# Performance work log

Measured on AMD Instinct MI355X. Metric: run time of the kernel, lower is better.

The kernel has to match this reference:

```python
import jax, jax.numpy as jnp
import numpy as np

E = 1024
H = 16
D = E // H  # projection_dim = 64


def setup_inputs() -> dict:
    key = jax.random.key(0)
    ks = jax.random.split(key, 9)
    s = 1.0 / np.sqrt(E)
    return {
        "inputs": jax.random.normal(ks[0], (2, 2048, E), dtype=jnp.float32),
        "Wq": jax.random.uniform(ks[1], (E, E), jnp.float32, -s, s),
        "bq": jax.random.uniform(ks[2], (E,), jnp.float32, -s, s),
        "Wk": jax.random.uniform(ks[3], (E, E), jnp.float32, -s, s),
        "bk": jax.random.uniform(ks[4], (E,), jnp.float32, -s, s),
        "Wv": jax.random.uniform(ks[5], (E, E), jnp.float32, -s, s),
        "bv": jax.random.uniform(ks[6], (E,), jnp.float32, -s, s),
        "Wo": jax.random.uniform(ks[7], (E, E), jnp.float32, -s, s),
        "bo": jax.random.uniform(ks[8], (E,), jnp.float32, -s, s),
    }


def reference(inputs, Wq, bq, Wk, bk, Wv, bv, Wo, bo):
    B, S, _ = inputs.shape
    # Linear layers use y = x @ W.T + b (torch convention); weights here stored as [E,E]
    q = inputs @ Wq.T + bq
    k = inputs @ Wk.T + bk
    v = inputs @ Wv.T + bv
    # separate heads: [B,S,E] -> [B,H,S,D]
    q = q.reshape(B, S, H, D).transpose(0, 2, 1, 3)
    k = k.reshape(B, S, H, D).transpose(0, 2, 1, 3)
    v = v.reshape(B, S, H, D).transpose(0, 2, 1, 3)
    scale = 1.0 / jnp.sqrt(jnp.float32(D))
    scores = jnp.einsum('bhqd,bhkd->bhqk', q, k) * scale  # [B,H,S,S]
    weights = jax.nn.softmax(scores, axis=-1)
    attn = jnp.einsum('bhqk,bhkd->bhqd', weights, v)  # [B,H,S,D]
    concat = attn.transpose(0, 2, 1, 3).reshape(B, S, E)
    # dropout is identity in eval mode
    return concat @ Wo.T + bo
```

## Files before the change

kernel.cpp:

```cpp
#include <hip/hip_runtime.h>
#include <hip/hip_bf16.h>
#include <stdint.h>

#define E_ 1024
#define H_ 16
#define D_ 64
#define B_ 2
#define S_ 2048
#define M_ 4096

typedef __bf16 bf16_t;
typedef __bf16 bf16x8 __attribute__((ext_vector_type(8)));
typedef __bf16 bf16x4 __attribute__((ext_vector_type(4)));
typedef __bf16 bf16x2 __attribute__((ext_vector_type(2)));
typedef float  f32x4  __attribute__((ext_vector_type(4)));
typedef float  f32x16 __attribute__((ext_vector_type(16)));
typedef unsigned int u32x2 __attribute__((ext_vector_type(2)));
typedef unsigned int u32x4 __attribute__((ext_vector_type(4)));

__global__ __launch_bounds__(256) void cvt_f32_to_bf16(const float* __restrict__ src,
                                                       bf16_t* __restrict__ dst, int n4) {
  int i = blockIdx.x * blockDim.x + threadIdx.x;
  if (i < n4) {
    float4 v = reinterpret_cast<const float4*>(src)[i];
    bf16x4 o;
    o[0] = (bf16_t)v.x; o[1] = (bf16_t)v.y; o[2] = (bf16_t)v.z; o[3] = (bf16_t)v.w;
    reinterpret_cast<bf16x4*>(dst)[i] = o;
  }
}

__global__ __launch_bounds__(256) void cvt_weights(
    const float* __restrict__ w0, const float* __restrict__ w1,
    const float* __restrict__ w2, const float* __restrict__ w3,
    bf16_t* __restrict__ d0, bf16_t* __restrict__ d1,
    bf16_t* __restrict__ d2, bf16_t* __restrict__ d3) {
  const int z = blockIdx.y;
  const float* src = (z == 0) ? w0 : (z == 1) ? w1 : (z == 2) ? w2 : w3;
  bf16_t* dst = (z == 0) ? d0 : (z == 1) ? d1 : (z == 2) ? d2 : d3;
  int i = blockIdx.x * blockDim.x + threadIdx.x;
  float4 v = reinterpret_cast<const float4*>(src)[i];
  bf16x4 o;
  o[0] = (bf16_t)v.x; o[1] = (bf16_t)v.y; o[2] = (bf16_t)v.z; o[3] = (bf16_t)v.w;
  reinterpret_cast<bf16x4*>(dst)[i] = o;
}

static __device__ __forceinline__ void gl_lds16(const bf16_t* g, bf16_t* l) {
  __builtin_amdgcn_global_load_lds((__attribute__((address_space(1))) void*)g,
                                   (__attribute__((address_space(3))) void*)l,
                                   16, 0, 0);
}

template <int SWAP>
static __device__ __forceinline__ void gemm128_mainloop(
    const bf16_t* __restrict__ Ag, const bf16_t* __restrict__ Bg,
    bf16_t* ldsA0, bf16_t* ldsA1, bf16_t* ldsB0, bf16_t* ldsB1,
    int m0, int n0, f32x4 acc[4][4]) {
  const int tid  = threadIdx.x;
  const int lane = tid & 63, wave = tid >> 6;
  const int lrow = lane & 15, lgrp = lane >> 4;
  const int wr = (wave >> 1) * 64, wc = (wave & 1) * 64;
  const int skol = (lane & 3) * 8;
  const int c0 = wave * 2;
  const int rowA = c0 * 16 + (lane >> 2);
  const f32x4 zero = {0.f, 0.f, 0.f, 0.f};
#pragma unroll
  for (int i = 0; i < 4; i++)
#pragma unroll
    for (int j = 0; j < 4; j++) acc[i][j] = zero;

  gl_lds16(Ag + (size_t)(m0 + rowA) * E_ + skol,      ldsA0 + c0 * 512);
  gl_lds16(Ag + (size_t)(m0 + rowA + 16) * E_ + skol, ldsA0 + (c0 + 1) * 512);
  gl_lds16(Bg + (size_t)(n0 + rowA) * E_ + skol,      ldsB0 + c0 * 512);
  gl_lds16(Bg + (size_t)(n0 + rowA + 16) * E_ + skol, ldsB0 + (c0 + 1) * 512);
  __syncthreads();

  for (int kt = 0; kt < E_ / 32; ++kt) {
    bf16_t* sA = (kt & 1) ? ldsA1 : ldsA0;
    bf16_t* sB = (kt & 1) ? ldsB1 : ldsB0;
    if (kt + 1 < E_ / 32) {
      bf16_t* dA = (kt & 1) ? ldsA0 : ldsA1;
      bf16_t* dB = (kt & 1) ? ldsB0 : ldsB1;
      const int k0 = (kt + 1) * 32;
      gl_lds16(Ag + (size_t)(m0 + rowA) * E_ + k0 + skol,      dA + c0 * 512);
      gl_lds16(Ag + (size_t)(m0 + rowA + 16) * E_ + k0 + skol, dA + (c0 + 1) * 512);
      gl_lds16(Bg + (size_t)(n0 + rowA) * E_ + k0 + skol,      dB + c0 * 512);
      gl_lds16(Bg + (size_t)(n0 + rowA + 16) * E_ + k0 + skol, dB + (c0 + 1) * 512);
    }
    bf16x8 fA[4], fB[4];
#pragma unroll
    for (int i = 0; i < 4; i++)
      fA[i] = *reinterpret_cast<const bf16x8*>(sA + (wr + i * 16 + lrow) * 32 + lgrp * 8);
#pragma unroll
    for (int j = 0; j < 4; j++)
      fB[j] = *reinterpret_cast<const bf16x8*>(sB + (wc + j * 16 + lrow) * 32 + lgrp * 8);
#pragma unroll
    for (int i = 0; i < 4; i++)
#pragma unroll
      for (int j = 0; j < 4; j++)
        acc[i][j] = SWAP
          ? __builtin_amdgcn_mfma_f32_16x16x32_bf16(fB[j], fA[i], acc[i][j], 0, 0, 0)
          : __builtin_amdgcn_mfma_f32_16x16x32_bf16(fA[i], fB[j], acc[i][j], 0, 0, 0);
    __syncthreads();
  }
}

__global__ __launch_bounds__(256) void qkv_gemm(
    const bf16_t* __restrict__ xbf,
    const bf16_t* __restrict__ Wqb, const bf16_t* __restrict__ Wkb, const bf16_t* __restrict__ Wvb,
    const float* __restrict__ bq, const float* __restrict__ bk, const float* __restrict__ bv,
    bf16_t* __restrict__ Qo, bf16_t* __restrict__ Ko, bf16_t* __restrict__ Vt) {
  __shared__ alignas(16) bf16_t ldsA[2][128 * 32];
  __shared__ alignas(16) bf16_t ldsB[2][128 * 32];
  const int z = blockIdx.z;
  const bf16_t* W   = (z == 0) ? Wqb : ((z == 1) ? Wkb : Wvb);
  const float* bias = (z == 0) ? bq  : ((z == 1) ? bk  : bv);
  const int m0 = blockIdx.x * 128, n0 = blockIdx.y * 128;
  const int lane = threadIdx.x & 63, wave = threadIdx.x >> 6;
  const int lrow = lane & 15, lgrp = lane >> 4;
  const int wr = (wave >> 1) * 64, wc = (wave & 1) * 64;
  f32x4 acc[4][4];

  if (z == 2) {
    gemm128_mainloop<0>(xbf, W, ldsA[0], ldsA[1], ldsB[0], ldsB[1], m0, n0, acc);
#pragma unroll
    for (int i = 0; i < 4; i++) {
      const int mbase = m0 + wr + i * 16 + lgrp * 4;
      const int b = mbase >> 11, s = mbase & (S_ - 1);
#pragma unroll
      for (int j = 0; j < 4; j++) {
        const int n = n0 + wc + j * 16 + lrow;
        const float bn = bias[n];
        const int h = n >> 6, d = n & 63;
        bf16x4 v;
#pragma unroll
        for (int r = 0; r < 4; r++) v[r] = (bf16_t)(acc[i][j][r] + bn);
        *reinterpret_cast<bf16x4*>(Vt + ((size_t)((b * H_ + h) * D_ + d)) * S_ + s) = v;
      }
    }
  } else {
    gemm128_mainloop<1>(xbf, W, ldsA[0], ldsA[1], ldsB[0], ldsB[1], m0, n0, acc);
    bf16_t* O = (z == 0) ? Qo : Ko;
    const float scale = (z == 0) ? 0.18033688011112042f : 1.0f;
#pragma unroll
    for (int i = 0; i < 4; i++) {
      const int m = m0 + wr + i * 16 + lrow;
      const int b = m >> 11, s = m & (S_ - 1);
#pragma unroll
      for (int j = 0; j < 4; j++) {
        const int nb = n0 + wc + j * 16 + lgrp * 4;
        const int h = nb >> 6, d = nb & 63;
        const f32x4 b4 = *reinterpret_cast<const f32x4*>(bias + nb);
        bf16x4 v;
#pragma unroll
        for (int r = 0; r < 4; r++) v[r] = (bf16_t)((acc[i][j][r] + b4[r]) * scale);
        *reinterpret_cast<bf16x4*>(O + ((size_t)((b * H_ + h) * S_) + s) * D_ + d) = v;
      }
    }
  }
}

__global__ __launch_bounds__(256) void out_gemm(
    const bf16_t* __restrict__ Cbf, const bf16_t* __restrict__ Wob,
    const float* __restrict__ bo, float* __restrict__ out) {
  __shared__ alignas(16) bf16_t ldsA[2][128 * 32];
  __shared__ alignas(16) bf16_t ldsB[2][128 * 32];
  const int m0 = blockIdx.x * 128, n0 = blockIdx.y * 128;
  f32x4 acc[4][4];
  gemm128_mainloop<1>(Cbf, Wob, ldsA[0], ldsA[1], ldsB[0], ldsB[1], m0, n0, acc);

  const int lane = threadIdx.x & 63, wave = threadIdx.x >> 6;
  const int lrow = lane & 15, lgrp = lane >> 4;
  const int wr = (wave >> 1) * 64, wc = (wave & 1) * 64;
#pragma unroll
  for (int i = 0; i < 4; i++) {
    const int m = m0 + wr + i * 16 + lrow;
#pragma unroll
    for (int j = 0; j < 4; j++) {
      const int nb = n0 + wc + j * 16 + lgrp * 4;
      const f32x4 b4 = *reinterpret_cast<const f32x4*>(bo + nb);
      f32x4 v = acc[i][j] + b4;
      *reinterpret_cast<f32x4*>(out + (size_t)m * E_ + nb) = v;
    }
  }
}


static __device__ __forceinline__ unsigned pack2(float a, float b) {
  bf16x2 t; t[0] = (bf16_t)a; t[1] = (bf16_t)b;
  return __builtin_bit_cast(unsigned, t);
}

static __device__ __forceinline__ bf16x8 mkfrag(unsigned a0, unsigned a1,
                                                unsigned a2, unsigned a3) {
  u32x2 s02 = __builtin_amdgcn_permlane32_swap(a0, a2, false, false);
  u32x2 s13 = __builtin_amdgcn_permlane32_swap(a1, a3, false, false);
  u32x4 t; t[0] = s02[0]; t[1] = s13[0]; t[2] = s02[1]; t[3] = s13[1];
  return *reinterpret_cast<bf16x8*>(&t);
}

__global__ __launch_bounds__(512) void attn_kernel(
    const bf16_t* __restrict__ Qg, const bf16_t* __restrict__ Kg,
    const bf16_t* __restrict__ Vtg, bf16_t* __restrict__ Og) {
  __shared__ alignas(16) bf16_t Kl[2][2][64 * 64];
  __shared__ alignas(16) bf16_t Vl[2][2][64 * 64];
  const int f = blockIdx.x;
  const int bh = (f & 7) * 4 + (f >> 7);
  const int q0 = ((f >> 3) & 15) * 128;
  const int tid = threadIdx.x, lane = tid & 63, wave = tid >> 6;
  const int qsub = wave & 3, kvg = wave >> 2;
  const int ql = lane & 31, hi = lane >> 5;
  const bf16_t* Qb = Qg + (size_t)bh * S_ * D_;
  const bf16_t* Kb = Kg + (size_t)bh * S_ * D_;
  const bf16_t* Vb = Vtg + (size_t)bh * D_ * S_;

  const int q = q0 + qsub * 32 + ql;
  bf16x8 qf[4];
#pragma unroll
  for (int ds = 0; ds < 4; ds++)
    qf[ds] = *reinterpret_cast<const bf16x8*>(Qb + (size_t)q * D_ + ds * 16 + hi * 8);

  f32x16 o0, o1;
#pragma unroll
  for (int r = 0; r < 16; r++) { o0[r] = 0.f; o1[r] = 0.f; }
  float li = 0.f;

  const int srow_lo = lane >> 3;
  const int sunit = lane & 7;

#pragma unroll
  for (int p = 0; p < 2; p++) {
    int c = p * 4 + qsub;
    int row = c * 8 + srow_lo;
    int u = sunit ^ (row & 7);
    gl_lds16(Kb + (size_t)(kvg * 64 + row) * D_ + u * 8, &Kl[kvg][0][c * 512]);
    gl_lds16(Vb + (size_t)row * S_ + kvg * 64 + u * 8, &Vl[kvg][0][c * 512]);
  }
  __syncthreads();

  for (int it = 0; it < S_ / 128; ++it) {
    const int cur = it & 1;
    if (it + 1 < S_ / 128) {
      const int kvn = (kvg + (it + 1) * 2) * 64;
#pragma unroll
      for (int p = 0; p < 2; p++) {
        int c = p * 4 + qsub;
        int row = c * 8 + srow_lo;
        int u = sunit ^ (row & 7);
        gl_lds16(Kb + (size_t)(kvn + row) * D_ + u * 8, &Kl[kvg][cur ^ 1][c * 512]);
        gl_lds16(Vb + (size_t)row * S_ + kvn + u * 8, &Vl[kvg][cur ^ 1][c * 512]);
      }
    }
    const char* kbuf = reinterpret_cast<const char*>(&Kl[kvg][cur][0]);
    const char* vbuf = reinterpret_cast<const char*>(&Vl[kvg][cur][0]);

    f32x16 pa0, pa1;
#pragma unroll
    for (int r = 0; r < 16; r++) { pa0[r] = 0.f; pa1[r] = 0.f; }
    __builtin_amdgcn_s_setprio(1);
#pragma unroll
    for (int ds = 0; ds < 4; ds++) {
      {
        const int krow = ql;
        const int u = (ds * 2 + hi) ^ (krow & 7);
        bf16x8 kf = *reinterpret_cast<const bf16x8*>(kbuf + krow * 128 + u * 16);
        pa0 = __builtin_amdgcn_mfma_f32_32x32x16_bf16(kf, qf[ds], pa0, 0, 0, 0);
      }
      {
        const int krow = 32 + ql;
        const int u = (ds * 2 + hi) ^ (krow & 7);
        bf16x8 kf = *reinterpret_cast<const bf16x8*>(kbuf + krow * 128 + u * 16);
        pa1 = __builtin_amdgcn_mfma_f32_32x32x16_bf16(kf, qf[ds], pa1, 0, 0, 0);
      }
    }
    __builtin_amdgcn_s_setprio(0);

    float ps = 0.f;
#pragma unroll
    for (int r = 0; r < 16; r++) {
      pa0[r] = __builtin_amdgcn_exp2f(pa0[r]); ps += pa0[r];
      pa1[r] = __builtin_amdgcn_exp2f(pa1[r]); ps += pa1[r];
    }
    {
      u32x2 ss = __builtin_amdgcn_permlane32_swap(
          __builtin_bit_cast(unsigned, ps), __builtin_bit_cast(unsigned, ps), false, false);
      ps = __builtin_bit_cast(float, ss[0]) + __builtin_bit_cast(float, ss[1]);
    }
    li += ps;

    unsigned w0[8], w1[8];
#pragma unroll
    for (int i = 0; i < 8; i++) {
      w0[i] = pack2(pa0[2 * i], pa0[2 * i + 1]);
      w1[i] = pack2(pa1[2 * i], pa1[2 * i + 1]);
    }
    bf16x8 bfr[4];
    bfr[0] = mkfrag(w0[0], w0[1], w0[2], w0[3]);
    bfr[1] = mkfrag(w0[4], w0[5], w0[6], w0[7]);
    bfr[2] = mkfrag(w1[0], w1[1], w1[2], w1[3]);
    bfr[3] = mkfrag(w1[4], w1[5], w1[6], w1[7]);

    __builtin_amdgcn_s_setprio(1);
#pragma unroll
    for (int step = 0; step < 4; step++) {
      {
        const int vrow = ql;
        const int u = (step * 2 + hi) ^ (vrow & 7);
        bf16x8 vf = *reinterpret_cast<const bf16x8*>(vbuf + vrow * 128 + u * 16);
        o0 = __builtin_amdgcn_mfma_f32_32x32x16_bf16(vf, bfr[step], o0, 0, 0, 0);
      }
      {
        const int vrow = 32 + ql;
        const int u = (step * 2 + hi) ^ (vrow & 7);
        bf16x8 vf = *reinterpret_cast<const bf16x8*>(vbuf + vrow * 128 + u * 16);
        o1 = __builtin_amdgcn_mfma_f32_32x32x16_bf16(vf, bfr[step], o1, 0, 0, 0);
      }
    }
    __builtin_amdgcn_s_setprio(0);

    __syncthreads();
  }

  f32x4* smO = reinterpret_cast<f32x4*>(&Kl[0][0][0]);
  float* smL = reinterpret_cast<float*>(&Vl[0][0][0]);
  const int mi_ = qsub * 64 + lane;
  if (kvg == 1) {
#pragma unroll
    for (int g = 0; g < 4; g++) {
      f32x4 a;
#pragma unroll
      for (int i = 0; i < 4; i++) a[i] = o0[g * 4 + i];
      smO[g * 256 + mi_] = a;
    }
#pragma unroll
    for (int g = 0; g < 4; g++) {
      f32x4 a;
#pragma unroll
      for (int i = 0; i < 4; i++) a[i] = o1[g * 4 + i];
      smO[(g + 4) * 256 + mi_] = a;
    }
    smL[mi_] = li;
  }
  __syncthreads();
  if (kvg == 0) {
    li += smL[mi_];
#pragma unroll
    for (int g = 0; g < 4; g++) {
      f32x4 a = smO[g * 256 + mi_];
#pragma unroll
      for (int i = 0; i < 4; i++) o0[g * 4 + i] += a[i];
    }
#pragma unroll
    for (int g = 0; g < 4; g++) {
      f32x4 a = smO[(g + 4) * 256 + mi_];
#pragma unroll
      for (int i = 0; i < 4; i++) o1[g * 4 + i] += a[i];
    }
    const float inv = 1.0f / li;
    const int b = bh >> 4, h = bh & 15;
    bf16_t* orow = Og + (size_t)(b * S_ + q) * E_ + h * 64;
#pragma unroll
    for (int g = 0; g < 4; g++) {
      bf16x4 v;
#pragma unroll
      for (int i = 0; i < 4; i++) v[i] = (bf16_t)(o0[g * 4 + i] * inv);
      *reinterpret_cast<bf16x4*>(orow + g * 8 + hi * 4) = v;
    }
#pragma unroll
    for (int g = 0; g < 4; g++) {
      bf16x4 v;
#pragma unroll
      for (int i = 0; i < 4; i++) v[i] = (bf16_t)(o1[g * 4 + i] * inv);
      *reinterpret_cast<bf16x4*>(orow + 32 + g * 8 + hi * 4) = v;
    }
  }
}

extern "C" void kernel_launch(void* const* d_in, const int* in_sizes, int n_in,
                              void* d_out, int out_size, void* d_ws, size_t ws_size,
                              hipStream_t stream) {
  (void)in_sizes; (void)n_in; (void)out_size; (void)ws_size;
  const float* x  = (const float*)d_in[0];
  const float* Wq = (const float*)d_in[1];
  const float* bq = (const float*)d_in[2];
  const float* Wk = (const float*)d_in[3];
  const float* bk = (const float*)d_in[4];
  const float* Wv = (const float*)d_in[5];
  const float* bv = (const float*)d_in[6];
  const float* Wo = (const float*)d_in[7];
  const float* bo = (const float*)d_in[8];
  float* out = (float*)d_out;

  bf16_t* ws  = (bf16_t*)d_ws;
  bf16_t* xbf = ws;
  bf16_t* Ct  = ws;
  bf16_t* wqb = ws + (4u << 20);
  bf16_t* wkb = ws + (5u << 20);
  bf16_t* wvb = ws + (6u << 20);
  bf16_t* wob = ws + (7u << 20);
  bf16_t* Qt  = ws + (8u << 20);
  bf16_t* Kt  = ws + (12u << 20);
  bf16_t* Vt  = ws + (16u << 20);

  cvt_f32_to_bf16<<<4096, 256, 0, stream>>>(x, xbf, 1 << 20);
  cvt_weights<<<dim3(1024, 4), 256, 0, stream>>>(Wq, Wk, Wv, Wo, wqb, wkb, wvb, wob);

  qkv_gemm<<<dim3(32, 8, 3), 256, 0, stream>>>(xbf, wqb, wkb, wvb, bq, bk, bv, Qt, Kt, Vt);
  attn_kernel<<<512, 512, 0, stream>>>(Qt, Kt, Vt, Ct);
  out_gemm<<<dim3(32, 8), 256, 0, stream>>>(Ct, wob, bo, out);
}
```

Baseline: 118.0 us.

## Replace QKV GEMM with 256x256-tile, 4-stage pipelined fused kernel

Replaces the 128x128 double-buffered QKV projection with a 512-thread kernel computing 256x256 tiles over the concatenated Wq/Wk/Wv weights. It uses a four-deep global-to-LDS prefetch ring with explicit vmcnt waits, XOR-swizzled LDS layout to avoid bank conflicts, and s_setprio around the MFMA block. The aim is higher data reuse per block and better overlap of loads with matrix math. The trade-offs are only 192 blocks, which may underfill the GPU, 128 KB of LDS per block, and Q/K outputs now written as scalar bf16 stores instead of 4-wide vectors.

```diff
diff --git a/kernel.cpp b/kernel.cpp
--- a/kernel.cpp
+++ b/kernel.cpp
@@ -50,6 +50,122 @@
                                    16, 0, 0);
 }
 
+__global__ __launch_bounds__(512) void qkv_gemm256(
+    const bf16_t* __restrict__ xbf, const bf16_t* __restrict__ Wqkv,
+    const float* __restrict__ bq, const float* __restrict__ bk, const float* __restrict__ bv,
+    bf16_t* __restrict__ Qo, bf16_t* __restrict__ Ko, bf16_t* __restrict__ Vt) {
+  __shared__ alignas(16) bf16_t lA[4][256 * 32];
+  __shared__ alignas(16) bf16_t lB[4][256 * 32];
+  const int tid = threadIdx.x, lane = tid & 63, wave = tid >> 6;
+  const int wr = wave >> 2, wc = wave & 3;
+  const int lrow = lane & 15, lgrp = lane >> 4;
+  const int m0 = blockIdx.x << 8, n0 = blockIdx.y << 8;
+
+  const int srow = tid >> 2;
+  const int scolg = (tid & 3) ^ ((srow >> 1) & 3);
+  const char* sA0 = (const char*)xbf  + (size_t)(m0 + srow) * 2048 + scolg * 16;
+  const char* sB0 = (const char*)Wqkv + (size_t)(n0 + srow) * 2048 + scolg * 16;
+
+  auto STAGE = [&](int T) {
+    const int buf = T & 3;
+    const char* a = sA0 + T * 64;
+    const char* b = sB0 + T * 64;
+    gl_lds16((const bf16_t*)a,                        &lA[buf][tid * 8]);
+    gl_lds16((const bf16_t*)(a + (size_t)128 * 2048), &lA[buf][4096 + tid * 8]);
+    gl_lds16((const bf16_t*)b,                        &lB[buf][tid * 8]);
+    gl_lds16((const bf16_t*)(b + (size_t)128 * 2048), &lB[buf][4096 + tid * 8]);
+  };
+
+  f32x4 acc[8][4];
+  const f32x4 zero = {0.f, 0.f, 0.f, 0.f};
+#pragma unroll
+  for (int i = 0; i < 8; i++)
+#pragma unroll
+    for (int j = 0; j < 4; j++) acc[i][j] = zero;
+
+  const int rswz = (lgrp ^ ((lrow >> 1) & 3)) * 16;
+  const int rdA = (wr * 128 + lrow) * 64 + rswz;
+  const int rdB = (wc * 64 + lrow) * 64 + rswz;
+
+  auto KTILE = [&](int T) {
+    const int buf = T & 3;
+    const char* kA = (const char*)&lA[buf][0] + rdA;
+    const char* kB = (const char*)&lB[buf][0] + rdB;
+    bf16x8 fA[8], fB[4];
+#pragma unroll
+    for (int i = 0; i < 8; i++) fA[i] = *reinterpret_cast<const bf16x8*>(kA + i * 1024);
+#pragma unroll
+    for (int j = 0; j < 4; j++) fB[j] = *reinterpret_cast<const bf16x8*>(kB + j * 1024);
+    __builtin_amdgcn_s_setprio(1);
+#pragma unroll
+    for (int i = 0; i < 8; i++)
+#pragma unroll
+      for (int j = 0; j < 4; j++)
+        acc[i][j] = __builtin_amdgcn_mfma_f32_16x16x32_bf16(fA[i], fB[j], acc[i][j], 0, 0, 0);
+    __builtin_amdgcn_s_setprio(0);
+  };
+
+  STAGE(0); STAGE(1); STAGE(2);
+  asm volatile("s_waitcnt vmcnt(8)" ::: "memory");
+  __builtin_amdgcn_s_barrier();
+  __builtin_amdgcn_sched_barrier(0);
+
+  for (int T = 0; T < 29; ++T) {
+    STAGE(T + 3);
+    KTILE(T);
+    asm volatile("s_waitcnt vmcnt(8)" ::: "memory");
+    __builtin_amdgcn_s_barrier();
+    __builtin_amdgcn_sched_barrier(0);
+  }
+  KTILE(29);
+  asm volatile("s_waitcnt vmcnt(4)" ::: "memory");
+  __builtin_amdgcn_s_barrier();
+  __builtin_amdgcn_sched_barrier(0);
+  KTILE(30);
+  asm volatile("s_waitcnt vmcnt(0)" ::: "memory");
+  __builtin_amdgcn_s_barrier();
+  __builtin_amdgcn_sched_barrier(0);
+  KTILE(31);
+
+  const int z = n0 >> 10;
+  const float* bias = (z == 0) ? bq : ((z == 1) ? bk : bv);
+  const int nloc_base = (n0 & 1023) + wc * 64;
+  if (z == 2) {
+#pragma unroll
+    for (int i = 0; i < 8; i++) {
+      const int mb = m0 + wr * 128 + i * 16 + lgrp * 4;
+      const int b_ = mb >> 11, s = mb & (S_ - 1);
+#pragma unroll
+      for (int j = 0; j < 4; j++) {
+        const int nl = nloc_base + j * 16 + lrow;
+        const float bn = bias[nl];
+        const int h = nl >> 6, d = nl & 63;
+        bf16x4 v;
+#pragma unroll
+        for (int r = 0; r < 4; r++) v[r] = (bf16_t)(acc[i][j][r] + bn);
+        *reinterpret_cast<bf16x4*>(Vt + ((size_t)((b_ * H_ + h) * D_ + d)) * S_ + s) = v;
+      }
+    }
+  } else {
+    bf16_t* O = z ? Ko : Qo;
+    const float scale = (z == 0) ? 0.18033688011112042f : 1.0f;
+#pragma unroll
+    for (int i = 0; i < 8; i++) {
+      const int mb = m0 + wr * 128 + i * 16 + lgrp * 4;
+      const int b_ = mb >> 11, s = mb & (S_ - 1);
+#pragma unroll
+      for (int j = 0; j < 4; j++) {
+        const int nl = nloc_base + j * 16 + lrow;
+        const float bn = bias[nl];
+        const int h = nl >> 6, d = nl & 63;
+#pragma unroll
+        for (int r = 0; r < 4; r++)
+          O[((size_t)((b_ * H_ + h) * S_) + (s + r)) * D_ + d] = (bf16_t)((acc[i][j][r] + bn) * scale);
+      }
+    }
+  }
+}
+
 template <int SWAP>
 static __device__ __forceinline__ void gemm128_mainloop(
     const bf16_t* __restrict__ Ag, const bf16_t* __restrict__ Bg,
@@ -101,61 +217,6 @@
           ? __builtin_amdgcn_mfma_f32_16x16x32_bf16(fB[j], fA[i], acc[i][j], 0, 0, 0)
           : __builtin_amdgcn_mfma_f32_16x16x32_bf16(fA[i], fB[j], acc[i][j], 0, 0, 0);
     __syncthreads();
-  }
-}
-
-__global__ __launch_bounds__(256) void qkv_gemm(
-    const bf16_t* __restrict__ xbf,
-    const bf16_t* __restrict__ Wqb, const bf16_t* __restrict__ Wkb, const bf16_t* __restrict__ Wvb,
-    const float* __restrict__ bq, const float* __restrict__ bk, const float* __restrict__ bv,
-    bf16_t* __restrict__ Qo, bf16_t* __restrict__ Ko, bf16_t* __restrict__ Vt) {
-  __shared__ alignas(16) bf16_t ldsA[2][128 * 32];
-  __shared__ alignas(16) bf16_t ldsB[2][128 * 32];
-  const int z = blockIdx.z;
-  const bf16_t* W   = (z == 0) ? Wqb : ((z == 1) ? Wkb : Wvb);
-  const float* bias = (z == 0) ? bq  : ((z == 1) ? bk  : bv);
-  const int m0 = blockIdx.x * 128, n0 = blockIdx.y * 128;
-  const int lane = threadIdx.x & 63, wave = threadIdx.x >> 6;
-  const int lrow = lane & 15, lgrp = lane >> 4;
-  const int wr = (wave >> 1) * 64, wc = (wave & 1) * 64;
-  f32x4 acc[4][4];
-
-  if (z == 2) {
-    gemm128_mainloop<0>(xbf, W, ldsA[0], ldsA[1], ldsB[0], ldsB[1], m0, n0, acc);
-#pragma unroll
-    for (int i = 0; i < 4; i++) {
-      const int mbase = m0 + wr + i * 16 + lgrp * 4;
-      const int b = mbase >> 11, s = mbase & (S_ - 1);
-#pragma unroll
-      for (int j = 0; j < 4; j++) {
-        const int n = n0 + wc + j * 16 + lrow;
-        const float bn = bias[n];
-        const int h = n >> 6, d = n & 63;
-        bf16x4 v;
-#pragma unroll
-        for (int r = 0; r < 4; r++) v[r] = (bf16_t)(acc[i][j][r] + bn);
-        *reinterpret_cast<bf16x4*>(Vt + ((size_t)((b * H_ + h) * D_ + d)) * S_ + s) = v;
-      }
-    }
-  } else {
-    gemm128_mainloop<1>(xbf, W, ldsA[0], ldsA[1], ldsB[0], ldsB[1], m0, n0, acc);
-    bf16_t* O = (z == 0) ? Qo : Ko;
-    const float scale = (z == 0) ? 0.18033688011112042f : 1.0f;
-#pragma unroll
-    for (int i = 0; i < 4; i++) {
-      const int m = m0 + wr + i * 16 + lrow;
-      const int b = m >> 11, s = m & (S_ - 1);
-#pragma unroll
-      for (int j = 0; j < 4; j++) {
-        const int nb = n0 + wc + j * 16 + lgrp * 4;
-        const int h = nb >> 6, d = nb & 63;
-        const f32x4 b4 = *reinterpret_cast<const f32x4*>(bias + nb);
-        bf16x4 v;
-#pragma unroll
-        for (int r = 0; r < 4; r++) v[r] = (bf16_t)((acc[i][j][r] + b4[r]) * scale);
-        *reinterpret_cast<bf16x4*>(O + ((size_t)((b * H_ + h) * S_) + s) * D_ + d) = v;
-      }
-    }
   }
 }
 
@@ -404,7 +465,7 @@
   cvt_f32_to_bf16<<<4096, 256, 0, stream>>>(x, xbf, 1 << 20);
   cvt_weights<<<dim3(1024, 4), 256, 0, stream>>>(Wq, Wk, Wv, Wo, wqb, wkb, wvb, wob);
 
-  qkv_gemm<<<dim3(32, 8, 3), 256, 0, stream>>>(xbf, wqb, wkb, wvb, bq, bk, bv, Qt, Kt, Vt);
+  qkv_gemm256<<<dim3(16, 12), 512, 0, stream>>>(xbf, wqb, bq, bk, bv, Qt, Kt, Vt);
   attn_kernel<<<512, 512, 0, stream>>>(Qt, Kt, Vt, Ct);
   out_gemm<<<dim3(32, 8), 256, 0, stream>>>(Ct, wob, bo, out);
 }
```

Measured after the change: 124.4 us. 1.05x slower.

## Merge QKV weights into one GEMM grid and compute softmax row sums via MFMA

Applied to the files above, without the earlier changes.

The QKV projection now treats Wq, Wk and Wv as a single contiguous 3072-row weight matrix. It launches a 2D grid where the N block index picks the output (Q, K or V), and the bias and head offsets are derived from the low bits of n0. In the attention kernel, the per-iteration exp-sum reduction (VALU adds plus a permlane swap) is replaced by an extra MFMA that multiplies a ones fragment by the probability fragments, so the row sum accumulates on the matrix unit. This adds a fifth MFMA per step and extra accumulator registers, which may affect occupancy, and it relies on the bf16-rounded probabilities for the denominator.

```diff
diff --git a/kernel.cpp b/kernel.cpp
--- a/kernel.cpp
+++ b/kernel.cpp
@@ -105,32 +105,30 @@
 }
 
 __global__ __launch_bounds__(256) void qkv_gemm(
-    const bf16_t* __restrict__ xbf,
-    const bf16_t* __restrict__ Wqb, const bf16_t* __restrict__ Wkb, const bf16_t* __restrict__ Wvb,
+    const bf16_t* __restrict__ xbf, const bf16_t* __restrict__ Wqkv,
     const float* __restrict__ bq, const float* __restrict__ bk, const float* __restrict__ bv,
     bf16_t* __restrict__ Qo, bf16_t* __restrict__ Ko, bf16_t* __restrict__ Vt) {
   __shared__ alignas(16) bf16_t ldsA[2][128 * 32];
   __shared__ alignas(16) bf16_t ldsB[2][128 * 32];
-  const int z = blockIdx.z;
-  const bf16_t* W   = (z == 0) ? Wqb : ((z == 1) ? Wkb : Wvb);
-  const float* bias = (z == 0) ? bq  : ((z == 1) ? bk  : bv);
   const int m0 = blockIdx.x * 128, n0 = blockIdx.y * 128;
+  const int z = n0 >> 10;
+  const float* bias = (z == 0) ? bq : ((z == 1) ? bk : bv);
   const int lane = threadIdx.x & 63, wave = threadIdx.x >> 6;
   const int lrow = lane & 15, lgrp = lane >> 4;
   const int wr = (wave >> 1) * 64, wc = (wave & 1) * 64;
   f32x4 acc[4][4];
 
   if (z == 2) {
-    gemm128_mainloop<0>(xbf, W, ldsA[0], ldsA[1], ldsB[0], ldsB[1], m0, n0, acc);
+    gemm128_mainloop<0>(xbf, Wqkv, ldsA[0], ldsA[1], ldsB[0], ldsB[1], m0, n0, acc);
 #pragma unroll
     for (int i = 0; i < 4; i++) {
       const int mbase = m0 + wr + i * 16 + lgrp * 4;
       const int b = mbase >> 11, s = mbase & (S_ - 1);
 #pragma unroll
       for (int j = 0; j < 4; j++) {
-        const int n = n0 + wc + j * 16 + lrow;
-        const float bn = bias[n];
-        const int h = n >> 6, d = n & 63;
+        const int nl = (n0 & 1023) + wc + j * 16 + lrow;
+        const float bn = bias[nl];
+        const int h = nl >> 6, d = nl & 63;
         bf16x4 v;
 #pragma unroll
         for (int r = 0; r < 4; r++) v[r] = (bf16_t)(acc[i][j][r] + bn);
@@ -138,7 +136,7 @@
       }
     }
   } else {
-    gemm128_mainloop<1>(xbf, W, ldsA[0], ldsA[1], ldsB[0], ldsB[1], m0, n0, acc);
+    gemm128_mainloop<1>(xbf, Wqkv, ldsA[0], ldsA[1], ldsB[0], ldsB[1], m0, n0, acc);
     bf16_t* O = (z == 0) ? Qo : Ko;
     const float scale = (z == 0) ? 0.18033688011112042f : 1.0f;
 #pragma unroll
@@ -147,7 +145,7 @@
       const int b = m >> 11, s = m & (S_ - 1);
 #pragma unroll
       for (int j = 0; j < 4; j++) {
-        const int nb = n0 + wc + j * 16 + lgrp * 4;
+        const int nb = (n0 & 1023) + wc + j * 16 + lgrp * 4;
         const int h = nb >> 6, d = nb & 63;
         const f32x4 b4 = *reinterpret_cast<const f32x4*>(bias + nb);
         bf16x4 v;
@@ -219,10 +217,13 @@
   for (int ds = 0; ds < 4; ds++)
     qf[ds] = *reinterpret_cast<const bf16x8*>(Qb + (size_t)q * D_ + ds * 16 + hi * 8);
 
-  f32x16 o0, o1;
-#pragma unroll
-  for (int r = 0; r < 16; r++) { o0[r] = 0.f; o1[r] = 0.f; }
-  float li = 0.f;
+  bf16x8 onesf;
+#pragma unroll
+  for (int i = 0; i < 8; i++) onesf[i] = (bf16_t)1.0f;
+
+  f32x16 o0, o1, oL;
+#pragma unroll
+  for (int r = 0; r < 16; r++) { o0[r] = 0.f; o1[r] = 0.f; oL[r] = 0.f; }
 
   const int srow_lo = lane >> 3;
   const int sunit = lane & 7;
@@ -274,18 +275,11 @@
     }
     __builtin_amdgcn_s_setprio(0);
 
-    float ps = 0.f;
 #pragma unroll
     for (int r = 0; r < 16; r++) {
-      pa0[r] = __builtin_amdgcn_exp2f(pa0[r]); ps += pa0[r];
-      pa1[r] = __builtin_amdgcn_exp2f(pa1[r]); ps += pa1[r];
-    }
-    {
-      u32x2 ss = __builtin_amdgcn_permlane32_swap(
-          __builtin_bit_cast(unsigned, ps), __builtin_bit_cast(unsigned, ps), false, false);
-      ps = __builtin_bit_cast(float, ss[0]) + __builtin_bit_cast(float, ss[1]);
-    }
-    li += ps;
+      pa0[r] = __builtin_amdgcn_exp2f(pa0[r]);
+      pa1[r] = __builtin_amdgcn_exp2f(pa1[r]);
+    }
 
     unsigned w0[8], w1[8];
 #pragma unroll
@@ -314,11 +308,14 @@
         bf16x8 vf = *reinterpret_cast<const bf16x8*>(vbuf + vrow * 128 + u * 16);
         o1 = __builtin_amdgcn_mfma_f32_32x32x16_bf16(vf, bfr[step], o1, 0, 0, 0);
       }
+      oL = __builtin_amdgcn_mfma_f32_32x32x16_bf16(onesf, bfr[step], oL, 0, 0, 0);
     }
     __builtin_amdgcn_s_setprio(0);
 
     __syncthreads();
   }
+
+  float li = oL[0];
 
   f32x4* smO = reinterpret_cast<f32x4*>(&Kl[0][0][0]);
   float* smL = reinterpret_cast<float*>(&Vl[0][0][0]);
@@ -404,7 +401,7 @@
   cvt_f32_to_bf16<<<4096, 256, 0, stream>>>(x, xbf, 1 << 20);
   cvt_weights<<<dim3(1024, 4), 256, 0, stream>>>(Wq, Wk, Wv, Wo, wqb, wkb, wvb, wob);
 
-  qkv_gemm<<<dim3(32, 8, 3), 256, 0, stream>>>(xbf, wqb, wkb, wvb, bq, bk, bv, Qt, Kt, Vt);
+  qkv_gemm<<<dim3(32, 24), 256, 0, stream>>>(xbf, wqb, bq, bk, bv, Qt, Kt, Vt);
   attn_kernel<<<512, 512, 0, stream>>>(Qt, Kt, Vt, Ct);
   out_gemm<<<dim3(32, 8), 256, 0, stream>>>(Ct, wob, bo, out);
 }
```

After: 127.7 us. 1.08x slower.
